# Kernel optimization log

Hardware: AMD Instinct MI355X
Metric: run time of the kernel (lower is better)

## Reference

```python
import jax, jax.numpy as jnp
import numpy as np

EPS = 1e-12  # torch F.normalize default eps


def setup_inputs() -> dict:
    key = jax.random.key(0)
    k1, k2, k3, k4 = jax.random.split(key, 4)
    N, F_IN, F_OUT = 8192, 128, 128
    x = jax.random.normal(k1, (N, F_IN), dtype=jnp.float32)
    adj = jax.random.uniform(k2, (N, N), dtype=jnp.float32)
    # fc_layer params (xavier_uniform with relu gain for W, default-ish bias)
    gain = float(np.sqrt(2.0))
    limit = gain * float(np.sqrt(6.0 / (F_IN + F_OUT)))
    W = jax.random.uniform(k3, (F_OUT, F_IN), dtype=jnp.float32, minval=-limit, maxval=limit)
    b = jax.random.uniform(k4, (F_OUT,), dtype=jnp.float32, minval=-1.0 / np.sqrt(F_IN), maxval=1.0 / np.sqrt(F_IN))
    return {"x": x, "adj": adj, "W": W, "b": b}


def reference(x, adj, W, b):
    N = adj.shape[0]
    # A' = A + I (self loops)
    a = adj + jnp.eye(N, dtype=adj.dtype)
    # degree normalization D^-1/2 A' D^-1/2 as a fused broadcast scale
    # (the torch code does this via two dense diag matmuls; same math)
    dinv = jax.lax.rsqrt(jnp.sum(a, axis=-1))  # [N]
    a = a * dinv[:, None] * dinv[None, :]
    # aggregation + linear
    h = a @ x                    # [N, F_IN]
    h = h @ W.T + b              # [N, F_OUT]
    # F.normalize(dim=1): L2 normalize each row
    norm = jnp.linalg.norm(h, axis=1, keepdims=True)
    return h / jnp.maximum(norm, EPS)
```

## Files before the change

kernel.cpp:

```cpp
#include <hip/hip_runtime.h>
#include <hip/hip_bf16.h>


typedef __attribute__((ext_vector_type(8))) short short8;
typedef __attribute__((ext_vector_type(4))) float f32x4;
typedef __attribute__((ext_vector_type(4))) unsigned short us4;

static __device__ __forceinline__ unsigned short f2bf(float f) {
    unsigned int u = __float_as_uint(f);
    u += 0x7FFFu + ((u >> 16) & 1u);
    return (unsigned short)(u >> 16);
}

__global__ __launch_bounds__(256) void gcn_prep(
    const float* __restrict__ adj, const float* __restrict__ x,
    const float* __restrict__ W,
    unsigned short* __restrict__ yT, float* __restrict__ dinv,
    unsigned short* __restrict__ Wb)
{
    const int tid = threadIdx.x;
    const int blk = blockIdx.x;
    if (blk >= 8192) {
        int idx = (blk - 8192) * 256 + tid;
        Wb[idx] = f2bf(W[idx]);
        return;
    }
    const long j = blk;
    const float4* row = (const float4*)(adj + j * 8192L);
    float s = 0.f;
#pragma unroll
    for (int it = 0; it < 8; ++it) {
        float4 v = row[it * 256 + tid];
        s += v.x + v.y + v.z + v.w;
    }
    for (int off = 1; off < 64; off <<= 1) s += __shfl_xor(s, off, 64);
    __shared__ float ps[4];
    __shared__ float sdi;
    if ((tid & 63) == 0) ps[tid >> 6] = s;
    __syncthreads();
    if (tid == 0) {
        float tot = ps[0] + ps[1] + ps[2] + ps[3] + 1.0f;
        float di = rsqrtf(tot);
        dinv[j] = di;
        sdi = di;
    }
    __syncthreads();
    if (tid < 128) {
        yT[(long)tid * 8192 + j] = f2bf(sdi * x[j * 128 + tid]);
    }
}

#define M_TILE 32
#define BKC    512
#define NCHUNK 16

__global__ __launch_bounds__(256, 1) void gcn_main(
    const float* __restrict__ adj, const float* __restrict__ x,
    const float* __restrict__ bias,
    const unsigned short* __restrict__ yT, const float* __restrict__ dinv,
    const unsigned short* __restrict__ Wb, float* __restrict__ out)
{
    __shared__ unsigned short Ab[2][M_TILE][BKC];

    const int tid  = threadIdx.x;
    const int wave = tid >> 6;
    const int lane = tid & 63;
    const int q    = lane >> 4;
    const int ln   = lane & 15;
    const int nb   = wave * 32;
    const long rowBase = (long)blockIdx.x * M_TILE;

    f32x4 acc[2][2] = {};
    float4 st[16];

    auto load_chunk = [&](int c) {
#pragma unroll
        for (int i = 0; i < 16; ++i) {
            int t   = wave * 16 + i;
            int row = t >> 1;
            int col = ((t & 1) << 8) + (lane << 2);
            st[i] = *(const float4*)&adj[(rowBase + row) * 8192L + (long)c * BKC + col];
        }
    };
    auto write_chunk = [&](int buf) {
#pragma unroll
        for (int i = 0; i < 16; ++i) {
            int t   = wave * 16 + i;
            int row = t >> 1;
            int col = ((t & 1) << 8) + (lane << 2);
            us4 w4;
            w4.x = f2bf(st[i].x); w4.y = f2bf(st[i].y);
            w4.z = f2bf(st[i].z); w4.w = f2bf(st[i].w);
            *(us4*)&Ab[buf][row][col] = w4;
        }
    };

    load_chunk(0);
    write_chunk(0);
    __syncthreads();

#pragma unroll 1
    for (int c = 0; c < NCHUNK; ++c) {
        const int cur = c & 1;
        if (c + 1 < NCHUNK) load_chunk(c + 1);
#pragma unroll 4
        for (int s = 0; s < BKC / 32; ++s) {
            const int k0 = s * 32 + q * 8;
            short8 a0 = *(const short8*)&Ab[cur][ln][k0];
            short8 a1 = *(const short8*)&Ab[cur][16 + ln][k0];
            const long kg = (long)c * BKC + k0;
            short8 b0 = *(const short8*)&yT[(nb + ln) * 8192L + kg];
            short8 b1 = *(const short8*)&yT[(nb + 16 + ln) * 8192L + kg];
            acc[0][0] = __builtin_amdgcn_mfma_f32_16x16x32_bf16(a0, b0, acc[0][0], 0, 0, 0);
            acc[0][1] = __builtin_amdgcn_mfma_f32_16x16x32_bf16(a0, b1, acc[0][1], 0, 0, 0);
            acc[1][0] = __builtin_amdgcn_mfma_f32_16x16x32_bf16(a1, b0, acc[1][0], 0, 0, 0);
            acc[1][1] = __builtin_amdgcn_mfma_f32_16x16x32_bf16(a1, b1, acc[1][1], 0, 0, 0);
        }
        if (c + 1 < NCHUNK) write_chunk(cur ^ 1);
        __syncthreads();
    }

    unsigned short* t_lds = &Ab[0][0][0];
    float* s_dinv = (float*)(t_lds + 32 * 136);
    float* s_part = s_dinv + 32;
    float* s_inv  = s_part + 128;

    if (tid < 32) s_dinv[tid] = dinv[rowBase + tid];
    __syncthreads();

#pragma unroll
    for (int mi = 0; mi < 2; ++mi)
#pragma unroll
        for (int nj = 0; nj < 2; ++nj)
#pragma unroll
            for (int r = 0; r < 4; ++r) {
                int m = mi * 16 + q * 4 + r;
                int n = nb + nj * 16 + ln;
                float di = s_dinv[m];
                float tv = di * acc[mi][nj][r] + di * di * x[(rowBase + m) * 128 + n];
                t_lds[m * 136 + n] = f2bf(tv);
            }
    __syncthreads();

    f32x4 z[2][2] = {};
#pragma unroll
    for (int s = 0; s < 4; ++s) {
        const int k0 = s * 32 + q * 8;
        short8 a0 = *(const short8*)&t_lds[ln * 136 + k0];
        short8 a1 = *(const short8*)&t_lds[(16 + ln) * 136 + k0];
        short8 b0 = *(const short8*)&Wb[(nb + ln) * 128 + k0];
        short8 b1 = *(const short8*)&Wb[(nb + 16 + ln) * 128 + k0];
        z[0][0] = __builtin_amdgcn_mfma_f32_16x16x32_bf16(a0, b0, z[0][0], 0, 0, 0);
        z[0][1] = __builtin_amdgcn_mfma_f32_16x16x32_bf16(a0, b1, z[0][1], 0, 0, 0);
        z[1][0] = __builtin_amdgcn_mfma_f32_16x16x32_bf16(a1, b0, z[1][0], 0, 0, 0);
        z[1][1] = __builtin_amdgcn_mfma_f32_16x16x32_bf16(a1, b1, z[1][1], 0, 0, 0);
    }

    float bv0 = bias[nb + ln], bv1 = bias[nb + 16 + ln];
    float zv[2][2][4];
    float rp[2][4];
#pragma unroll
    for (int mi = 0; mi < 2; ++mi)
#pragma unroll
        for (int r = 0; r < 4; ++r) {
            float v0 = z[mi][0][r] + bv0;
            float v1 = z[mi][1][r] + bv1;
            zv[mi][0][r] = v0; zv[mi][1][r] = v1;
            rp[mi][r] = v0 * v0 + v1 * v1;
        }
#pragma unroll
    for (int mi = 0; mi < 2; ++mi)
#pragma unroll
        for (int r = 0; r < 4; ++r)
            for (int off = 1; off < 16; off <<= 1)
                rp[mi][r] += __shfl_xor(rp[mi][r], off, 64);
    if (ln == 0) {
#pragma unroll
        for (int mi = 0; mi < 2; ++mi)
#pragma unroll
            for (int r = 0; r < 4; ++r)
                s_part[(mi * 16 + q * 4 + r) * 4 + wave] = rp[mi][r];
    }
    __syncthreads();
    if (tid < 32) {
        float s = s_part[tid * 4] + s_part[tid * 4 + 1] + s_part[tid * 4 + 2] + s_part[tid * 4 + 3];
        float nrm = sqrtf(s);
        s_inv[tid] = 1.0f / fmaxf(nrm, 1e-12f);
    }
    __syncthreads();

#pragma unroll
    for (int mi = 0; mi < 2; ++mi)
#pragma unroll
        for (int nj = 0; nj < 2; ++nj)
#pragma unroll
            for (int r = 0; r < 4; ++r) {
                int m = mi * 16 + q * 4 + r;
                int n = nb + nj * 16 + ln;
                out[(rowBase + m) * 128 + n] = zv[mi][nj][r] * s_inv[m];
            }
}

extern "C" void kernel_launch(void* const* d_in, const int* in_sizes, int n_in,
                              void* d_out, int out_size, void* d_ws, size_t ws_size,
                              hipStream_t stream) {
    const float* x   = (const float*)d_in[0];
    const float* adj = (const float*)d_in[1];
    const float* W   = (const float*)d_in[2];
    const float* b   = (const float*)d_in[3];
    float* out = (float*)d_out;

    unsigned short* yT  = (unsigned short*)d_ws;
    float*          dv  = (float*)((char*)d_ws + (2u << 20));
    unsigned short* Wb  = (unsigned short*)((char*)d_ws + (2u << 20) + 32768);

    gcn_prep<<<8192 + 64, 256, 0, stream>>>(adj, x, W, yT, dv, Wb);
    gcn_main<<<256, 256, 0, stream>>>(adj, x, b, yT, dv, Wb, out);
}
```

Before: 473.7 us.

## Widen prep and main kernels to 512 threads with per-wave row and column splits

The prep kernel now handles 32 adjacency rows per block, one wave per 4 rows, instead of one row per 256-thread block. Its yT writes are coalesced along j, which should cut launch count and the scattered transposed stores. The main kernel doubles to 8 waves, each owning 16 output columns instead of 32, so more waves per CU can hide adj streaming latency. The cost is fewer MFMAs per A-fragment LDS load and an extra norm-reduction stage across 8 waves.

```diff
diff --git a/kernel.cpp b/kernel.cpp
--- a/kernel.cpp
+++ b/kernel.cpp
@@ -12,7 +12,7 @@
     return (unsigned short)(u >> 16);
 }
 
-__global__ __launch_bounds__(256) void gcn_prep(
+__global__ __launch_bounds__(512) void gcn_prep(
     const float* __restrict__ adj, const float* __restrict__ x,
     const float* __restrict__ W,
     unsigned short* __restrict__ yT, float* __restrict__ dinv,
@@ -20,33 +20,39 @@
 {
     const int tid = threadIdx.x;
     const int blk = blockIdx.x;
-    if (blk >= 8192) {
-        int idx = (blk - 8192) * 256 + tid;
+    if (blk >= 256) {
+        int idx = (blk - 256) * 512 + tid;
         Wb[idx] = f2bf(W[idx]);
         return;
     }
-    const long j = blk;
-    const float4* row = (const float4*)(adj + j * 8192L);
-    float s = 0.f;
-#pragma unroll
-    for (int it = 0; it < 8; ++it) {
-        float4 v = row[it * 256 + tid];
-        s += v.x + v.y + v.z + v.w;
-    }
-    for (int off = 1; off < 64; off <<= 1) s += __shfl_xor(s, off, 64);
-    __shared__ float ps[4];
-    __shared__ float sdi;
-    if ((tid & 63) == 0) ps[tid >> 6] = s;
-    __syncthreads();
-    if (tid == 0) {
-        float tot = ps[0] + ps[1] + ps[2] + ps[3] + 1.0f;
-        float di = rsqrtf(tot);
-        dinv[j] = di;
-        sdi = di;
-    }
-    __syncthreads();
-    if (tid < 128) {
-        yT[(long)tid * 8192 + j] = f2bf(sdi * x[j * 128 + tid]);
+    const int wave = tid >> 6;
+    const int lane = tid & 63;
+    const long j0 = (long)blk * 32;
+
+    __shared__ float s_di[32];
+
+    for (int r = 0; r < 4; ++r) {
+        const long j = j0 + wave * 4 + r;
+        const float4* row = (const float4*)(adj + j * 8192L);
+        float s = 0.f;
+#pragma unroll
+        for (int it = 0; it < 32; ++it) {
+            float4 v = row[it * 64 + lane];
+            s += (v.x + v.y) + (v.z + v.w);
+        }
+        for (int off = 1; off < 64; off <<= 1) s += __shfl_xor(s, off, 64);
+        if (lane == 0) s_di[wave * 4 + r] = rsqrtf(s + 1.0f);
+    }
+    __syncthreads();
+    if (tid < 32) dinv[j0 + tid] = s_di[tid];
+
+    const int jj = tid & 31;
+    const int fb = tid >> 5;
+    const float di = s_di[jj];
+#pragma unroll
+    for (int p = 0; p < 8; ++p) {
+        int f = p * 16 + fb;
+        yT[(long)f * 8192 + j0 + jj] = f2bf(di * x[(j0 + jj) * 128 + f]);
     }
 }
 
@@ -54,7 +60,7 @@
 #define BKC    512
 #define NCHUNK 16
 
-__global__ __launch_bounds__(256, 1) void gcn_main(
+__global__ __launch_bounds__(512, 1) void gcn_main(
     const float* __restrict__ adj, const float* __restrict__ x,
     const float* __restrict__ bias,
     const unsigned short* __restrict__ yT, const float* __restrict__ dinv,
@@ -67,16 +73,16 @@
     const int lane = tid & 63;
     const int q    = lane >> 4;
     const int ln   = lane & 15;
-    const int nb   = wave * 32;
+    const int nb   = wave * 16;
     const long rowBase = (long)blockIdx.x * M_TILE;
 
-    f32x4 acc[2][2] = {};
-    float4 st[16];
+    f32x4 acc[2] = {};
+    float4 st[8];
 
     auto load_chunk = [&](int c) {
 #pragma unroll
-        for (int i = 0; i < 16; ++i) {
-            int t   = wave * 16 + i;
+        for (int i = 0; i < 8; ++i) {
+            int t   = wave * 8 + i;
             int row = t >> 1;
             int col = ((t & 1) << 8) + (lane << 2);
             st[i] = *(const float4*)&adj[(rowBase + row) * 8192L + (long)c * BKC + col];
@@ -84,8 +90,8 @@
     };
     auto write_chunk = [&](int buf) {
 #pragma unroll
-        for (int i = 0; i < 16; ++i) {
-            int t   = wave * 16 + i;
+        for (int i = 0; i < 8; ++i) {
+            int t   = wave * 8 + i;
             int row = t >> 1;
             int col = ((t & 1) << 8) + (lane << 2);
             us4 w4;
@@ -110,11 +116,8 @@
             short8 a1 = *(const short8*)&Ab[cur][16 + ln][k0];
             const long kg = (long)c * BKC + k0;
             short8 b0 = *(const short8*)&yT[(nb + ln) * 8192L + kg];
-            short8 b1 = *(const short8*)&yT[(nb + 16 + ln) * 8192L + kg];
-            acc[0][0] = __builtin_amdgcn_mfma_f32_16x16x32_bf16(a0, b0, acc[0][0], 0, 0, 0);
-            acc[0][1] = __builtin_amdgcn_mfma_f32_16x16x32_bf16(a0, b1, acc[0][1], 0, 0, 0);
-            acc[1][0] = __builtin_amdgcn_mfma_f32_16x16x32_bf16(a1, b0, acc[1][0], 0, 0, 0);
-            acc[1][1] = __builtin_amdgcn_mfma_f32_16x16x32_bf16(a1, b1, acc[1][1], 0, 0, 0);
+            acc[0] = __builtin_amdgcn_mfma_f32_16x16x32_bf16(a0, b0, acc[0], 0, 0, 0);
+            acc[1] = __builtin_amdgcn_mfma_f32_16x16x32_bf16(a1, b0, acc[1], 0, 0, 0);
         }
         if (c + 1 < NCHUNK) write_chunk(cur ^ 1);
         __syncthreads();
@@ -123,7 +126,7 @@
     unsigned short* t_lds = &Ab[0][0][0];
     float* s_dinv = (float*)(t_lds + 32 * 136);
     float* s_part = s_dinv + 32;
-    float* s_inv  = s_part + 128;
+    float* s_inv  = s_part + 256;
 
     if (tid < 32) s_dinv[tid] = dinv[rowBase + tid];
     __syncthreads();
@@ -131,42 +134,36 @@
 #pragma unroll
     for (int mi = 0; mi < 2; ++mi)
 #pragma unroll
-        for (int nj = 0; nj < 2; ++nj)
-#pragma unroll
-            for (int r = 0; r < 4; ++r) {
-                int m = mi * 16 + q * 4 + r;
-                int n = nb + nj * 16 + ln;
-                float di = s_dinv[m];
-                float tv = di * acc[mi][nj][r] + di * di * x[(rowBase + m) * 128 + n];
-                t_lds[m * 136 + n] = f2bf(tv);
-            }
-    __syncthreads();
-
-    f32x4 z[2][2] = {};
+        for (int r = 0; r < 4; ++r) {
+            int m = mi * 16 + q * 4 + r;
+            int n = nb + ln;
+            float di = s_dinv[m];
+            float tv = di * acc[mi][r] + di * di * x[(rowBase + m) * 128 + n];
+            t_lds[m * 136 + n] = f2bf(tv);
+        }
+    __syncthreads();
+
+    f32x4 z[2] = {};
 #pragma unroll
     for (int s = 0; s < 4; ++s) {
         const int k0 = s * 32 + q * 8;
         short8 a0 = *(const short8*)&t_lds[ln * 136 + k0];
         short8 a1 = *(const short8*)&t_lds[(16 + ln) * 136 + k0];
         short8 b0 = *(const short8*)&Wb[(nb + ln) * 128 + k0];
-        short8 b1 = *(const short8*)&Wb[(nb + 16 + ln) * 128 + k0];
-        z[0][0] = __builtin_amdgcn_mfma_f32_16x16x32_bf16(a0, b0, z[0][0], 0, 0, 0);
-        z[0][1] = __builtin_amdgcn_mfma_f32_16x16x32_bf16(a0, b1, z[0][1], 0, 0, 0);
-        z[1][0] = __builtin_amdgcn_mfma_f32_16x16x32_bf16(a1, b0, z[1][0], 0, 0, 0);
-        z[1][1] = __builtin_amdgcn_mfma_f32_16x16x32_bf16(a1, b1, z[1][1], 0, 0, 0);
-    }
-
-    float bv0 = bias[nb + ln], bv1 = bias[nb + 16 + ln];
-    float zv[2][2][4];
+        z[0] = __builtin_amdgcn_mfma_f32_16x16x32_bf16(a0, b0, z[0], 0, 0, 0);
+        z[1] = __builtin_amdgcn_mfma_f32_16x16x32_bf16(a1, b0, z[1], 0, 0, 0);
+    }
+
+    float bv0 = bias[nb + ln];
+    float zv[2][4];
     float rp[2][4];
 #pragma unroll
     for (int mi = 0; mi < 2; ++mi)
 #pragma unroll
         for (int r = 0; r < 4; ++r) {
-            float v0 = z[mi][0][r] + bv0;
-            float v1 = z[mi][1][r] + bv1;
-            zv[mi][0][r] = v0; zv[mi][1][r] = v1;
-            rp[mi][r] = v0 * v0 + v1 * v1;
+            float v0 = z[mi][r] + bv0;
+            zv[mi][r] = v0;
+            rp[mi][r] = v0 * v0;
         }
 #pragma unroll
     for (int mi = 0; mi < 2; ++mi)
@@ -179,11 +176,13 @@
         for (int mi = 0; mi < 2; ++mi)
 #pragma unroll
             for (int r = 0; r < 4; ++r)
-                s_part[(mi * 16 + q * 4 + r) * 4 + wave] = rp[mi][r];
+                s_part[(mi * 16 + q * 4 + r) * 8 + wave] = rp[mi][r];
     }
     __syncthreads();
     if (tid < 32) {
-        float s = s_part[tid * 4] + s_part[tid * 4 + 1] + s_part[tid * 4 + 2] + s_part[tid * 4 + 3];
+        float s = 0.f;
+#pragma unroll
+        for (int w = 0; w < 8; ++w) s += s_part[tid * 8 + w];
         float nrm = sqrtf(s);
         s_inv[tid] = 1.0f / fmaxf(nrm, 1e-12f);
     }
@@ -192,13 +191,11 @@
 #pragma unroll
     for (int mi = 0; mi < 2; ++mi)
 #pragma unroll
-        for (int nj = 0; nj < 2; ++nj)
-#pragma unroll
-            for (int r = 0; r < 4; ++r) {
-                int m = mi * 16 + q * 4 + r;
-                int n = nb + nj * 16 + ln;
-                out[(rowBase + m) * 128 + n] = zv[mi][nj][r] * s_inv[m];
-            }
+        for (int r = 0; r < 4; ++r) {
+            int m = mi * 16 + q * 4 + r;
+            int n = nb + ln;
+            out[(rowBase + m) * 128 + n] = zv[mi][r] * s_inv[m];
+        }
 }
 
 extern "C" void kernel_launch(void* const* d_in, const int* in_sizes, int n_in,
@@ -214,6 +211,6 @@
     float*          dv  = (float*)((char*)d_ws + (2u << 20));
     unsigned short* Wb  = (unsigned short*)((char*)d_ws + (2u << 20) + 32768);
 
-    gcn_prep<<<8192 + 64, 256, 0, stream>>>(adj, x, W, yT, dv, Wb);
-    gcn_main<<<256, 256, 0, stream>>>(adj, x, b, yT, dv, Wb, out);
-}
+    gcn_prep<<<256 + 32, 512, 0, stream>>>(adj, x, W, yT, dv, Wb);
+    gcn_main<<<256, 512, 0, stream>>>(adj, x, b, yT, dv, Wb, out);
+}
```

Measured after the change: 471.5 us. Within noise of the previous version (-0.5%).
